# Kernel tuning notes

Measured on AMD Instinct MI355X. Metric: run time of the kernel, lower is better.

Reference implementation:

```python
import jax, jax.numpy as jnp
import numpy as np

B, L, D = 2, 4096, 1024
H, DK, DV = 4, 256, 256
CONV_K = 4
FIR_KS = (1, 3, 7, 15)
GQP = 128
NS = len(FIR_KS) + 2  # fir scales + delta path + direct value path
GIN = GQP + NS
GH = max(8, GIN)
CHUNK = 32
FLOOR = 0.02  # step 0 -> floor_start


def l2norm(x):
    return x * jax.lax.rsqrt(jnp.sum(x * x, -1, keepdims=True) + 1e-6)


def dw_causal_conv(x, w):
    # x: (B, L, C), w: (C, K) depthwise causal conv (ShortConvolution / FIR)
    K = w.shape[1]
    y = jax.lax.conv_general_dilated(
        jnp.moveaxis(x, 1, 2), w[:, None, :], (1,), [(K - 1, 0)],
        feature_group_count=w.shape[0],
        dimension_numbers=("NCH", "OIH", "NCH"))
    return jnp.moveaxis(y, 1, 2)


def delta_rule_chunkwise(q, k, v, beta):
    # q,k: (b,h,L,dk)  v: (b,h,L,dv)  beta: (b,h,L);  L % CHUNK == 0
    b, h, Lp, dk = q.shape
    dv = v.shape[-1]
    n = Lp // CHUNK
    q = l2norm(q)
    k = l2norm(k)
    v = v * beta[..., None]
    kb = k * beta[..., None]
    rs = lambda t: t.reshape(b, h, n, CHUNK, -1)
    q, k, v, kb = rs(q), rs(k), rs(v), rs(kb)
    tri = jnp.triu(jnp.ones((CHUNK, CHUNK), bool), 0)       # incl diag
    tri_s = jnp.triu(jnp.ones((CHUNK, CHUNK), bool), 1)     # strict upper
    # inv = -(k_beta k^T) masked to strictly-lower
    inv = -jnp.where(tri, 0.0, jnp.einsum('bhncd,bhned->bhnce', kb, k))
    # forward substitution: (I - A)^{-1} - I for strictly lower A
    for i in range(1, CHUNK):
        row = inv[:, :, :, i, :]                              # (b,h,n,C)
        upd = jnp.einsum('bhnk,bhnkj->bhnj', row, inv)        # zero for j>=i
        inv = inv.at[:, :, :, i, :].add(upd)
    inv = inv + jnp.eye(CHUNK, dtype=inv.dtype)
    inv = inv.astype(jnp.bfloat16).astype(q.dtype)
    u = inv @ v                                               # (b,h,n,C,dv)
    w = inv @ kb                                              # (b,h,n,C,dk)
    mv = lambda t: jnp.moveaxis(t, 2, 0)                      # -> (n,b,h,C,d)
    S0 = jnp.zeros((b, h, dk, dv), q.dtype)

    def step(S, xs):
        q_i, k_i, u_i, w_i = xs
        attn = jnp.where(tri_s, 0.0, q_i @ jnp.swapaxes(k_i, -1, -2))
        u_t = u_i - w_i @ S
        o = q_i @ S + attn @ u_t
        S = S + jnp.swapaxes(k_i, -1, -2) @ u_t
        return S, o

    _, out = jax.lax.scan(step, S0, (mv(q), mv(k), mv(u), mv(w)))
    return jnp.moveaxis(out, 0, 2).reshape(b, h, Lp, dv)


def rmsnorm(x, w, eps=1e-5):
    return x * jax.lax.rsqrt(jnp.mean(x * x, -1, keepdims=True) + eps) * w


def _dirac_fir(key, channels, k):
    w = jnp.zeros((channels, k), jnp.float32).at[:, -1].set(1.0)
    return w + 0.01 * jax.random.normal(key, (channels, k), jnp.float32)


def setup_inputs():
    key = jax.random.key(0)
    ks = jax.random.split(key, 24)
    sc = 0.02
    C = H * DV
    b2 = jnp.zeros((NS,), jnp.float32).at[-1].set(1.0)  # identity-path bias
    return {
        "hidden_states": jax.random.normal(ks[0], (B, L, D), jnp.float32),
        "Wq": jax.random.normal(ks[1], (D, H * DK), jnp.float32) * sc,
        "Wk": jax.random.normal(ks[2], (D, H * DK), jnp.float32) * sc,
        "Wv": jax.random.normal(ks[3], (D, H * DV), jnp.float32) * sc,
        "Wb": jax.random.normal(ks[4], (D, H), jnp.float32) * sc,
        "conv_q_w": jax.random.normal(ks[5], (H * DK, CONV_K), jnp.float32) * 0.1,
        "conv_k_w": jax.random.normal(ks[6], (H * DK, CONV_K), jnp.float32) * 0.1,
        "conv_v_w": jax.random.normal(ks[7], (H * DV, CONV_K), jnp.float32) * 0.1,
        "fir_w0": _dirac_fir(ks[8], C, FIR_KS[0]),
        "fir_w1": _dirac_fir(ks[9], C, FIR_KS[1]),
        "fir_w2": _dirac_fir(ks[10], C, FIR_KS[2]),
        "fir_w3": _dirac_fir(ks[11], C, FIR_KS[3]),
        "Wqg": jax.random.normal(ks[12], (D, GQP), jnp.float32) * sc,
        "bqg": jnp.zeros((GQP,), jnp.float32),
        "Wf1": jax.random.normal(ks[13], (GIN, GH), jnp.float32) * sc,
        "bf1": jnp.zeros((GH,), jnp.float32),
        "Wf2": jax.random.normal(ks[14], (GH, NS), jnp.float32) * sc,
        "bf2": b2,
        "log_temp": jnp.zeros((H,), jnp.float32),
        "o_norm_w": jnp.ones((DV,), jnp.float32),
        "Wo": jax.random.normal(ks[15], (H * DV, D), jnp.float32) * sc,
    }


def reference(hidden_states, Wq, Wk, Wv, Wb, conv_q_w, conv_k_w, conv_v_w,
              fir_w0, fir_w1, fir_w2, fir_w3, Wqg, bqg, Wf1, bf1, Wf2, bf2,
              log_temp, o_norm_w, Wo):
    x = hidden_states
    # projections + causal ShortConvolution with SiLU (qk_activation='silu')
    q = jax.nn.silu(dw_causal_conv(x @ Wq, conv_q_w))
    k = jax.nn.silu(dw_causal_conv(x @ Wk, conv_k_w))
    v = jax.nn.silu(dw_causal_conv(x @ Wv, conv_v_w))
    q = q.reshape(B, L, H, DK)
    k = k.reshape(B, L, H, DK)
    v_direct = v.reshape(B, L, H, DV)
    beta = jax.nn.sigmoid(x @ Wb)  # (B,L,H)
    bh = lambda t: jnp.swapaxes(t, 1, 2)  # (B,L,H,d) -> (B,H,L,d)
    delta_bh = delta_rule_chunkwise(bh(q), bh(k), bh(v_direct), jnp.swapaxes(beta, 1, 2))
    delta_out = jnp.swapaxes(delta_bh, 1, 2)  # (B,L,H,DV)
    # multi-scale depthwise causal FIR branches on the value stream
    v_flat = v_direct.reshape(B, L, H * DV)
    firs = [dw_causal_conv(v_flat, w).reshape(B, L, H, DV)
            for w in (fir_w0, fir_w1, fir_w2, fir_w3)]
    streams = jnp.stack(firs + [delta_out, v_direct], axis=3)  # (B,L,H,NS,DV)
    # query-conditioned summary router
    summaries = jnp.mean(streams, axis=-1)                     # (B,L,H,NS)
    qg = x @ Wqg + bqg                                         # (B,L,GQP)
    qg = jnp.broadcast_to(qg[:, :, None, :], (B, L, H, GQP))
    gate_in = jnp.concatenate([qg, summaries], axis=-1)        # (B,L,H,GIN)
    hmid = jax.nn.gelu(gate_in @ Wf1 + bf1, approximate=False)
    logits = (hmid @ Wf2 + bf2) / jnp.exp(log_temp)[None, None, :, None]
    p = jax.nn.softmax(logits, axis=-1)
    p = p * (1.0 - NS * FLOOR) + FLOOR                          # prob floor
    fused = jnp.einsum('blhs,blhsd->blhd', p, streams)
    o = rmsnorm(fused, o_norm_w)
    return o.reshape(B, L, H * DV) @ Wo
```

## Files before the change

kernel.cpp:

```cpp
#include <hip/hip_runtime.h>
#include <hip/hip_bf16.h>
#include <math.h>

#define B_ 2
#define L_ 4096
#define D_ 1024
#define H_ 4
#define DK_ 256
#define BL_ 8192
#define C_ 1024
#define NCH_ 128
#define GQP_c 128
#define NS_c 6
#define GIN_c 134
#define GH_c 134

typedef __attribute__((ext_vector_type(8))) short short8;
typedef __attribute__((ext_vector_type(4))) float f32x4;

__device__ __forceinline__ float block_sum256(float v, float* red) {
  int t = threadIdx.x;
  #pragma unroll
  for (int o = 32; o > 0; o >>= 1) v += __shfl_down(v, o, 64);
  __syncthreads();
  if ((t & 63) == 0) red[t >> 6] = v;
  __syncthreads();
  return red[0] + red[1] + red[2] + red[3];
}

__device__ __forceinline__ unsigned short bf16bits(float f) {
  __hip_bfloat16 h = __float2bfloat16(f);
  return *(unsigned short*)&h;
}

__device__ __forceinline__ float bits2f(unsigned short u) {
  unsigned int x = ((unsigned int)u) << 16;
  return *(float*)&x;
}

__device__ __forceinline__ float4 fma4(float4 a, float4 b, float4 c) {
  return make_float4(fmaf(a.x, b.x, c.x), fmaf(a.y, b.y, c.y),
                     fmaf(a.z, b.z, c.z), fmaf(a.w, b.w, c.w));
}

__device__ __forceinline__ void gload_lds16(const void* g, void* l) {
  __builtin_amdgcn_global_load_lds(
      (const __attribute__((address_space(1))) void*)g,
      (__attribute__((address_space(3))) void*)l, 16, 0, 0);
}

__global__ __launch_bounds__(256) void f32_to_bf16_k(const float* __restrict__ in,
    __hip_bfloat16* __restrict__ out) {
  size_t i = ((size_t)blockIdx.x * 256 + threadIdx.x) << 2;
  float4 v = *(const float4*)(in + i);
  ushort4 o;
  o.x = bf16bits(v.x); o.y = bf16bits(v.y); o.z = bf16bits(v.z); o.w = bf16bits(v.w);
  *(ushort4*)((unsigned short*)out + i) = o;
}

__global__ __launch_bounds__(256) void transpose_bf16(const float* __restrict__ W,
    __hip_bfloat16* __restrict__ WT, int K, int N) {
  __shared__ float tile[32][33];
  int t = threadIdx.x;
  int r = t >> 3, c4 = (t & 7) << 2;
  int n0 = blockIdx.x << 5, k0 = blockIdx.y << 5;
  float4 v = *(const float4*)(W + (size_t)(k0 + r) * N + n0 + c4);
  tile[r][c4] = v.x; tile[r][c4 + 1] = v.y; tile[r][c4 + 2] = v.z; tile[r][c4 + 3] = v.w;
  __syncthreads();
  ushort4 o;
  o.x = bf16bits(tile[c4][r]);
  o.y = bf16bits(tile[c4 + 1][r]);
  o.z = bf16bits(tile[c4 + 2][r]);
  o.w = bf16bits(tile[c4 + 3][r]);
  *(ushort4*)((unsigned short*)WT + (size_t)(n0 + r) * K + k0 + c4) = o;
}

__global__ __launch_bounds__(256) void small_transpose(const float* __restrict__ in,
    float* __restrict__ out, int R, int Cc, int OS) {
  int total = Cc * OS;
  for (int e = blockIdx.x * 256 + threadIdx.x; e < total; e += gridDim.x * 256) {
    int cIdx = e / OS, r = e - cIdx * OS;
    out[e] = (r < R) ? in[(size_t)r * Cc + cIdx] : 0.f;
  }
}

__global__ __launch_bounds__(256) void wf1q_prep(const float* __restrict__ Wf1,
    __hip_bfloat16* __restrict__ out) {
  int idx = blockIdx.x * 256 + threadIdx.x;
  int u = idx >> 7, i = idx & 127;
  float val = (u < GH_c) ? Wf1[i * GH_c + u] : 0.f;
  out[idx] = __float2bfloat16(val);
}

__global__ __launch_bounds__(256) void gemm_bf16(
    const __hip_bfloat16* __restrict__ A, const __hip_bfloat16* __restrict__ BT,
    const float* __restrict__ bias, float* __restrict__ C, int M, int N, int K) {
  __shared__ __align__(16) __hip_bfloat16 Asm[4096];
  __shared__ __align__(16) __hip_bfloat16 Bsm[4096];
  int tid = threadIdx.x;
  int lane = tid & 63, wave = tid >> 6;
  int wm = wave >> 1, wn = wave & 1;
  int rowBase = blockIdx.y * 128, colBase = blockIdx.x * 128;
  f32x4 acc[4][4];
  #pragma unroll
  for (int i = 0; i < 4; ++i)
    #pragma unroll
    for (int j = 0; j < 4; ++j) acc[i][j] = (f32x4){0.f, 0.f, 0.f, 0.f};

  for (int kt = 0; kt < K; kt += 32) {
    __syncthreads();
    #pragma unroll
    for (int it = 0; it < 2; ++it) {
      int s = tid + (it << 8);
      int T = s >> 6, q = (s >> 4) & 3, m = s & 15;
      const __hip_bfloat16* ga = A + (size_t)(rowBase + T * 16 + m) * K + kt + q * 8;
      gload_lds16(ga, Asm + s * 8);
      const __hip_bfloat16* gb = BT + (size_t)(colBase + T * 16 + m) * K + kt + q * 8;
      gload_lds16(gb, Bsm + s * 8);
    }
    __syncthreads();
    short8 af[4], bfr[4];
    #pragma unroll
    for (int i = 0; i < 4; ++i) {
      af[i]  = *(const short8*)(Asm + ((wm * 4 + i) << 9) + lane * 8);
      bfr[i] = *(const short8*)(Bsm + ((wn * 4 + i) << 9) + lane * 8);
    }
    #pragma unroll
    for (int i = 0; i < 4; ++i)
      #pragma unroll
      for (int j = 0; j < 4; ++j)
        acc[i][j] = __builtin_amdgcn_mfma_f32_16x16x32_bf16(af[i], bfr[j], acc[i][j], 0, 0, 0);
  }
  int r0 = (lane >> 4) * 4, c0 = lane & 15;
  #pragma unroll
  for (int i = 0; i < 4; ++i) {
    int row = rowBase + (wm * 4 + i) * 16 + r0;
    #pragma unroll
    for (int j = 0; j < 4; ++j) {
      int col = colBase + (wn * 4 + j) * 16 + c0;
      float bs = bias ? bias[col] : 0.f;
      #pragma unroll
      for (int r = 0; r < 4; ++r)
        C[(size_t)(row + r) * N + col] = acc[i][j][r] + bs;
    }
  }
}

__global__ __launch_bounds__(256) void conv_silu(const float* __restrict__ in,
    const float* __restrict__ w, float* __restrict__ out) {
  int idx = blockIdx.x * 256 + threadIdx.x;
  int c = idx & (C_ - 1);
  int l = (idx >> 10) & (L_ - 1);
  float acc = 0.f;
  #pragma unroll
  for (int j = 0; j < 4; ++j) {
    int ll = l - 3 + j;
    if (ll >= 0) acc += w[(c << 2) + j] * in[idx + ((j - 3) << 10)];
  }
  out[idx] = acc / (1.f + expf(-acc));
}

__global__ __launch_bounds__(256) void beta_kernel(const float* __restrict__ x,
    const float* __restrict__ Wb, float* __restrict__ beta) {
  int row = blockIdx.x;
  int t = threadIdx.x;
  int h = t >> 6, lane = t & 63;
  const float* xr = x + (size_t)row * D_;
  float acc = 0.f;
  for (int k = lane; k < D_; k += 64) acc += xr[k] * Wb[(k << 2) + h];
  #pragma unroll
  for (int o = 32; o > 0; o >>= 1) acc += __shfl_down(acc, o, 64);
  if (lane == 0) beta[(row << 2) + h] = 1.f / (1.f + expf(-acc));
}

__global__ __launch_bounds__(256) void precompute(const float* __restrict__ q,
    const float* __restrict__ k, const float* __restrict__ v,
    const float* __restrict__ beta,
    float* __restrict__ qn, float* __restrict__ kn,
    float* __restrict__ vb, float* __restrict__ kb) {
  __shared__ float red[4];
  int bid = blockIdx.x;
  int t = threadIdx.x;
  int b = bid >> 14;
  int h = (bid >> 12) & 3;
  int l = bid & (L_ - 1);
  size_t in_off = (((size_t)(b * L_ + l)) << 10) + (h << 8) + t;
  float qv = q[in_off], kv = k[in_off], vv = v[in_off];
  float sq = block_sum256(qv * qv, red);
  float sk = block_sum256(kv * kv, red);
  float rq = rsqrtf(sq + 1e-6f);
  float rk = rsqrtf(sk + 1e-6f);
  float bt = beta[((b * L_ + l) << 2) + h];
  size_t oo = ((size_t)bid << 8) + t;
  float knv = kv * rk;
  qn[oo] = qv * rq;
  kn[oo] = knv;
  vb[oo] = vv * bt;
  kb[oo] = knv * bt;
}

__global__ __launch_bounds__(256) void inv_attn(const float* __restrict__ qn,
    const float* kn, const float* __restrict__ kb,
    float* __restrict__ invb, __hip_bfloat16* __restrict__ att_bf,
    __hip_bfloat16* knT_bf) {
  __shared__ float kn_s[32][257];
  __shared__ float inv_s[32][33];
  int ci = blockIdx.x;
  int t = threadIdx.x;
  size_t base = ((size_t)ci) << 13;
  for (int e = t; e < 8192; e += 256) kn_s[e >> 8][e & 255] = kn[base + e];
  __syncthreads();
  {
    unsigned short tmp[32];
    #pragma unroll
    for (int j = 0; j < 32; ++j) tmp[j] = bf16bits(kn_s[j][t]);
    unsigned short* kd = (unsigned short*)knT_bf + (((size_t)ci) << 14) +
                         (size_t)(t >> 4) * 512 + (size_t)(t & 15) * 8;
    #pragma unroll
    for (int g = 0; g < 4; ++g) *(uint4*)(kd + g * 128) = ((const uint4*)tmp)[g];
  }
  {
    int r = t >> 3, kt = t & 7;
    const float4* qrow = (const float4*)(qn + base + (size_t)r * 256 + (kt << 5));
    unsigned short tmp[32];
    #pragma unroll
    for (int i = 0; i < 8; ++i) {
      float4 f = qrow[i];
      tmp[i * 4 + 0] = bf16bits(f.x); tmp[i * 4 + 1] = bf16bits(f.y);
      tmp[i * 4 + 2] = bf16bits(f.z); tmp[i * 4 + 3] = bf16bits(f.w);
    }
    unsigned short* qd = (unsigned short*)knT_bf + (((size_t)ci) << 14) + 8192 +
                         (size_t)(((r >> 4) << 3) + kt) * 512 + (size_t)(r & 15) * 8;
    #pragma unroll
    for (int g = 0; g < 4; ++g) *(uint4*)(qd + g * 128) = ((const uint4*)tmp)[g];
  }
  #pragma unroll
  for (int p = 0; p < 4; ++p) {
    int e = t + (p << 8);
    int i = e >> 5, j = e & 31;
    const float* kbi = kb + base + (i << 8);
    const float* qni = qn + base + (i << 8);
    float am = 0.f, aa = 0.f;
    for (int kk = 0; kk < 256; ++kk) {
      float knv = kn_s[j][kk];
      am += kbi[kk] * knv;
      aa += qni[kk] * knv;
    }
    inv_s[i][j] = (j < i) ? -am : 0.f;
    ((unsigned short*)att_bf)[((size_t)ci << 10) + (size_t)(i >> 4) * 512 +
        (size_t)((i & 15) + ((j >> 3) << 4)) * 8 + (j & 7)] =
        bf16bits((j <= i) ? aa : 0.f);
  }
  __syncthreads();
  for (int i = 1; i < 32; ++i) {
    float upd = 0.f;
    if (t < i) {
      for (int kk = t + 1; kk < i; ++kk) upd += inv_s[i][kk] * inv_s[kk][t];
    }
    __syncthreads();
    if (t < i) inv_s[i][t] += upd;
    __syncthreads();
  }
  #pragma unroll
  for (int p = 0; p < 4; ++p) {
    int e = t + (p << 8);
    int i = e >> 5, j = e & 31;
    float val = inv_s[i][j] + (i == j ? 1.f : 0.f);
    val = __bfloat162float(__float2bfloat16(val));
    invb[((size_t)ci << 10) + e] = val;
  }
}

__global__ __launch_bounds__(256) void uw_kernel(const float* __restrict__ invb,
    float* __restrict__ vb_u, float* kb_w, __hip_bfloat16* w_bf) {
  __shared__ float inv_s[32][33];
  __shared__ float tile[32][260];
  int ci = blockIdx.x, t = threadIdx.x;
  size_t base = ((size_t)ci) << 13;
  for (int e = t; e < 1024; e += 256) inv_s[e >> 5][e & 31] = invb[((size_t)ci << 10) + e];
  for (int ph = 0; ph < 2; ++ph) {
    const float* src = (ph == 0) ? vb_u : kb_w;
    __syncthreads();
    for (int f = t; f < 2048; f += 256) {
      int e = f << 2;
      *(float4*)&tile[e >> 8][e & 255] = *(const float4*)(src + base + e);
    }
    __syncthreads();
    int c4 = (t & 63) << 2;
    int ig = t >> 6;
    float4 acc[8];
    #pragma unroll
    for (int ii = 0; ii < 8; ++ii) acc[ii] = make_float4(0.f, 0.f, 0.f, 0.f);
    for (int j = 0; j < 32; ++j) {
      float4 v4 = *(const float4*)&tile[j][c4];
      #pragma unroll
      for (int ii = 0; ii < 8; ++ii) {
        float iv = inv_s[(ig << 3) + ii][j];
        acc[ii].x += iv * v4.x; acc[ii].y += iv * v4.y;
        acc[ii].z += iv * v4.z; acc[ii].w += iv * v4.w;
      }
    }
    #pragma unroll
    for (int ii = 0; ii < 8; ++ii) {
      int i = (ig << 3) + ii;
      if (ph == 0) {
        *(float4*)(vb_u + base + (i << 8) + c4) = acc[ii];
      } else {
        ushort4 o;
        o.x = bf16bits(-acc[ii].x); o.y = bf16bits(-acc[ii].y);
        o.z = bf16bits(-acc[ii].z); o.w = bf16bits(-acc[ii].w);
        unsigned short* wd = (unsigned short*)w_bf + (((size_t)ci) << 14) +
            (size_t)(((i >> 4) << 3) + (c4 >> 5)) * 512 +
            (size_t)((i & 15) + (((c4 >> 3) & 3) << 4)) * 8 + (c4 & 7);
        *(ushort4*)wd = o;
      }
    }
  }
}

__global__ __launch_bounds__(128, 1) void scan_kernel(
    const __hip_bfloat16* __restrict__ w_bf,
    const __hip_bfloat16* __restrict__ kq_bf,
    const __hip_bfloat16* __restrict__ att_bf,
    const float* __restrict__ u, float* __restrict__ dout) {
  __shared__ __align__(16) unsigned short stg[2][25600];
  __shared__ __align__(16) unsigned short Shi[16 * 264];
  __shared__ __align__(16) unsigned short Slo[16 * 264];
  __shared__ __align__(16) float UtT[16 * 36];
  int tid = threadIdx.x;
  int wave = tid >> 6, lane = tid & 63;
  int mlane = lane & 15, quad = lane >> 4;
  int bh = blockIdx.x & 7;
  int cb = blockIdx.x >> 3;
  int cbase = cb << 4;

  const unsigned short* wbase = (const unsigned short*)w_bf;
  const unsigned short* kqbase = (const unsigned short*)kq_bf;
  const unsigned short* abase = (const unsigned short*)att_bf;

  auto stage_chunk = [&](int nc, int buf) {
    size_t ci = (size_t)(bh * NCH_ + nc);
    const unsigned short* wg = wbase + (ci << 14) + lane * 8;
    const unsigned short* kg = kqbase + (ci << 14) + lane * 8;
    const unsigned short* qg = kqbase + (ci << 14) + 8192 + lane * 8;
    const unsigned short* ag = abase + (ci << 10) + lane * 8;
    unsigned short* l = &stg[buf][lane * 8];
    #pragma unroll
    for (int s = 0; s < 16; ++s) {
      gload_lds16(wg + s * 512, l + s * 512);
      gload_lds16(kg + s * 512, l + 8192 + s * 512);
      gload_lds16(qg + s * 512, l + 16384 + s * 512);
    }
    gload_lds16(ag, l + 24576);
    gload_lds16(ag + 512, l + 25088);
  };
  float ur[8], urn[8];
  auto load_u8 = [&](int nc, float* dst) {
    size_t cbf = ((size_t)(bh * NCH_ + nc)) << 13;
    const float* up = u + cbf + (size_t)(quad * 4) * 256 + cbase + mlane;
    #pragma unroll
    for (int tt = 0; tt < 2; ++tt)
      #pragma unroll
      for (int r = 0; r < 4; ++r) dst[tt * 4 + r] = up[(tt * 16 + r) * 256];
  };

  f32x4 accS[16];
  if (wave == 1) {
    stage_chunk(0, 0);
    asm volatile("s_waitcnt vmcnt(0)" ::: "memory");
  } else {
    for (int e = lane; e < 16 * 264; e += 64) { Shi[e] = 0; Slo[e] = 0; }
    #pragma unroll
    for (int i = 0; i < 16; ++i) accS[i] = (f32x4){0.f, 0.f, 0.f, 0.f};
    load_u8(0, ur);
  }
  __syncthreads();

  for (int nc = 0; nc < NCH_; ++nc) {
    int cur = nc & 1;
    if (wave == 1) {
      if (nc + 1 < NCH_) stage_chunk(nc + 1, cur ^ 1);
      asm volatile("s_waitcnt vmcnt(0)" ::: "memory");
    } else {
      int nn = nc + 1 < NCH_ ? nc + 1 : NCH_ - 1;
      const unsigned short* SW = &stg[cur][0];
      const unsigned short* SK = &stg[cur][8192];
      const unsigned short* SQ = &stg[cur][16384];
      const unsigned short* SA = &stg[cur][24576];

      f32x4 uh0 = (f32x4){ur[0], ur[1], ur[2], ur[3]};
      f32x4 uh1 = (f32x4){ur[4], ur[5], ur[6], ur[7]};
      f32x4 ul0 = (f32x4){0.f, 0.f, 0.f, 0.f}, ul1 = (f32x4){0.f, 0.f, 0.f, 0.f};
      f32x4 oh0 = (f32x4){0.f, 0.f, 0.f, 0.f}, oh1 = (f32x4){0.f, 0.f, 0.f, 0.f};
      f32x4 ol0 = (f32x4){0.f, 0.f, 0.f, 0.f}, ol1 = (f32x4){0.f, 0.f, 0.f, 0.f};
      #pragma unroll
      for (int kt = 0; kt < 8; ++kt) {
        short8 bhi = *(const short8*)&Shi[mlane * 264 + kt * 32 + quad * 8];
        short8 blo = *(const short8*)&Slo[mlane * 264 + kt * 32 + quad * 8];
        short8 w0 = *(const short8*)&SW[kt * 512 + lane * 8];
        short8 w1 = *(const short8*)&SW[(8 + kt) * 512 + lane * 8];
        short8 q0 = *(const short8*)&SQ[kt * 512 + lane * 8];
        short8 q1 = *(const short8*)&SQ[(8 + kt) * 512 + lane * 8];
        uh0 = __builtin_amdgcn_mfma_f32_16x16x32_bf16(w0, bhi, uh0, 0, 0, 0);
        ul0 = __builtin_amdgcn_mfma_f32_16x16x32_bf16(w0, blo, ul0, 0, 0, 0);
        uh1 = __builtin_amdgcn_mfma_f32_16x16x32_bf16(w1, bhi, uh1, 0, 0, 0);
        ul1 = __builtin_amdgcn_mfma_f32_16x16x32_bf16(w1, blo, ul1, 0, 0, 0);
        oh0 = __builtin_amdgcn_mfma_f32_16x16x32_bf16(q0, bhi, oh0, 0, 0, 0);
        ol0 = __builtin_amdgcn_mfma_f32_16x16x32_bf16(q0, blo, ol0, 0, 0, 0);
        oh1 = __builtin_amdgcn_mfma_f32_16x16x32_bf16(q1, bhi, oh1, 0, 0, 0);
        ol1 = __builtin_amdgcn_mfma_f32_16x16x32_bf16(q1, blo, ol1, 0, 0, 0);
      }
      f32x4 ut0 = uh0 + ul0, ut1 = uh1 + ul1;
      *(f32x4*)&UtT[mlane * 36 + quad * 4] = ut0;
      *(f32x4*)&UtT[mlane * 36 + 16 + quad * 4] = ut1;
      load_u8(nn, urn);
      short8 but;
      {
        const float* up = &UtT[mlane * 36 + quad * 8];
        #pragma unroll
        for (int j = 0; j < 8; ++j) but[j] = (short)bf16bits(up[j]);
      }
      short8 a0 = *(const short8*)&SA[lane * 8];
      short8 a1 = *(const short8*)&SA[512 + lane * 8];
      f32x4 o0 = oh0 + ol0, o1 = oh1 + ol1;
      o0 = __builtin_amdgcn_mfma_f32_16x16x32_bf16(a0, but, o0, 0, 0, 0);
      o1 = __builtin_amdgcn_mfma_f32_16x16x32_bf16(a1, but, o1, 0, 0, 0);
      size_t cbf = ((size_t)(bh * NCH_ + nc)) << 13;
      float* op = dout + cbf + (size_t)(quad * 4) * 256 + cbase + mlane;
      #pragma unroll
      for (int r = 0; r < 4; ++r) { op[r * 256] = o0[r]; op[(16 + r) * 256] = o1[r]; }
      #pragma unroll
      for (int t2 = 0; t2 < 16; ++t2) {
        short8 kA = *(const short8*)&SK[t2 * 512 + lane * 8];
        accS[t2] = __builtin_amdgcn_mfma_f32_16x16x32_bf16(kA, but, accS[t2], 0, 0, 0);
        unsigned short nh[4], nl[4];
        #pragma unroll
        for (int r = 0; r < 4; ++r) {
          float sv = accS[t2][r];
          unsigned short hb = bf16bits(sv);
          nh[r] = hb;
          nl[r] = bf16bits(sv - bits2f(hb));
        }
        *(uint2*)&Shi[mlane * 264 + t2 * 16 + quad * 4] = *(const uint2*)nh;
        *(uint2*)&Slo[mlane * 264 + t2 * 16 + quad * 4] = *(const uint2*)nl;
      }
      #pragma unroll
      for (int r = 0; r < 8; ++r) ur[r] = urn[r];
    }
    __syncthreads();
  }
}

__global__ __launch_bounds__(256, 1) void gate_kernel(
    const float* __restrict__ v, const float* __restrict__ delta,
    const float* __restrict__ qgH,
    const float* __restrict__ fw0, const float* __restrict__ fw1T,
    const float* __restrict__ fw2T, const float* __restrict__ fw3T,
    const float* __restrict__ Wf1, const float* __restrict__ Wf2,
    const float* __restrict__ bf1, const float* __restrict__ bf2,
    const float* __restrict__ ltm, const float* __restrict__ onw,
    __hip_bfloat16* __restrict__ obf) {
  __shared__ float W1t[6][136];
  __shared__ float W2f[804];
  __shared__ float bf1s[136];
  int t = threadIdx.x;
  int wave = t >> 6, lane = t & 63;
  for (int e = t; e < 804; e += 256) {
    int s = e / 134, u = e - s * 134;
    W1t[s][u] = Wf1[(128 + s) * GH_c + u];
    W2f[e] = Wf2[e];
  }
  if (t < GH_c) bf1s[t] = bf1[t];
  __syncthreads();

  int bid = blockIdx.x;
  int bl0 = (((bid & 7) << 7) | (bid >> 3)) << 3;
  int b = bl0 >> 12;
  int h = wave;
  int c = (h << 8) + (lane << 2);

  float4 fw3r[15], fw2r[7], fw1r[3], fw0r;
  #pragma unroll
  for (int j = 0; j < 15; ++j) fw3r[j] = *(const float4*)(fw3T + (j << 10) + c);
  #pragma unroll
  for (int j = 0; j < 7; ++j) fw2r[j] = *(const float4*)(fw2T + (j << 10) + c);
  #pragma unroll
  for (int j = 0; j < 3; ++j) fw1r[j] = *(const float4*)(fw1T + (j << 10) + c);
  fw0r = *(const float4*)(fw0 + c);
  float4 ow = *(const float4*)(onw + (lane << 2));
  float itemp = expf(ltm[h]);
  float b2r[6];
  #pragma unroll
  for (int s = 0; s < 6; ++s) b2r[s] = bf2[s];
  int u3 = 128 + (lane < 6 ? lane : 0);

  auto gelu = [](float a) -> float {
    return 0.5f * a * (1.f + erff(a * 0.70710678f));
  };

  for (int tk = 0; tk < 8; ++tk) {
    int bl = bl0 + tk;
    int l = bl & (L_ - 1);
    float4 st0, st1, st2, st3, st4, st5;
    st1 = make_float4(0, 0, 0, 0);
    st2 = make_float4(0, 0, 0, 0);
    st3 = make_float4(0, 0, 0, 0);
    #pragma unroll
    for (int j = 0; j < 15; ++j) {
      int ll = l - 14 + j;
      float4 vj = make_float4(0, 0, 0, 0);
      if (ll >= 0) vj = *(const float4*)(v + ((((size_t)(b * L_ + ll)) << 10) + c));
      st3 = fma4(fw3r[j], vj, st3);
      if (j >= 8) st2 = fma4(fw2r[j - 8], vj, st2);
      if (j >= 12) st1 = fma4(fw1r[j - 12], vj, st1);
      if (j == 14) {
        st0 = make_float4(fw0r.x * vj.x, fw0r.y * vj.y, fw0r.z * vj.z, fw0r.w * vj.w);
        st5 = vj;
      }
    }
    st4 = *(const float4*)(delta + ((((size_t)((b * H_ + h) * L_ + l)) << 8) + (lane << 2)));

    float s0 = st0.x + st0.y + st0.z + st0.w;
    float s1 = st1.x + st1.y + st1.z + st1.w;
    float s2 = st2.x + st2.y + st2.z + st2.w;
    float s3 = st3.x + st3.y + st3.z + st3.w;
    float s4 = st4.x + st4.y + st4.z + st4.w;
    float s5 = st5.x + st5.y + st5.z + st5.w;
    #pragma unroll
    for (int o = 32; o > 0; o >>= 1) {
      s0 += __shfl_down(s0, o, 64); s1 += __shfl_down(s1, o, 64);
      s2 += __shfl_down(s2, o, 64); s3 += __shfl_down(s3, o, 64);
      s4 += __shfl_down(s4, o, 64); s5 += __shfl_down(s5, o, 64);
    }
    float ss_[6];
    ss_[0] = __shfl(s0, 0, 64) * (1.f / 256.f);
    ss_[1] = __shfl(s1, 0, 64) * (1.f / 256.f);
    ss_[2] = __shfl(s2, 0, 64) * (1.f / 256.f);
    ss_[3] = __shfl(s3, 0, 64) * (1.f / 256.f);
    ss_[4] = __shfl(s4, 0, 64) * (1.f / 256.f);
    ss_[5] = __shfl(s5, 0, 64) * (1.f / 256.f);

    const float* qr = qgH + ((size_t)bl << 8);
    float a0 = qr[lane] + bf1s[lane];
    float a1 = qr[64 + lane] + bf1s[64 + lane];
    float a2 = qr[u3] + bf1s[u3];
    #pragma unroll
    for (int s = 0; s < 6; ++s) {
      a0 = fmaf(W1t[s][lane], ss_[s], a0);
      a1 = fmaf(W1t[s][64 + lane], ss_[s], a1);
      a2 = fmaf(W1t[s][u3], ss_[s], a2);
    }
    float h0 = gelu(a0);
    float h1 = gelu(a1);
    float h2 = (lane < 6) ? gelu(a2) : 0.f;

    const float* w2a = W2f + lane * 6;
    const float* w2b = W2f + (64 + lane) * 6;
    const float* w2c = W2f + u3 * 6;
    float t0 = h0 * w2a[0] + h1 * w2b[0] + h2 * w2c[0];
    float t1 = h0 * w2a[1] + h1 * w2b[1] + h2 * w2c[1];
    float t2 = h0 * w2a[2] + h1 * w2b[2] + h2 * w2c[2];
    float t3 = h0 * w2a[3] + h1 * w2b[3] + h2 * w2c[3];
    float t4 = h0 * w2a[4] + h1 * w2b[4] + h2 * w2c[4];
    float t5 = h0 * w2a[5] + h1 * w2b[5] + h2 * w2c[5];
    #pragma unroll
    for (int o = 32; o > 0; o >>= 1) {
      t0 += __shfl_down(t0, o, 64); t1 += __shfl_down(t1, o, 64);
      t2 += __shfl_down(t2, o, 64); t3 += __shfl_down(t3, o, 64);
      t4 += __shfl_down(t4, o, 64); t5 += __shfl_down(t5, o, 64);
    }
    float p0, p1, p2, p3, p4, p5;
    if (lane == 0) {
      float l0v = (t0 + b2r[0]) / itemp, l1v = (t1 + b2r[1]) / itemp;
      float l2v = (t2 + b2r[2]) / itemp, l3v = (t3 + b2r[3]) / itemp;
      float l4v = (t4 + b2r[4]) / itemp, l5v = (t5 + b2r[5]) / itemp;
      float m = fmaxf(fmaxf(fmaxf(l0v, l1v), fmaxf(l2v, l3v)), fmaxf(l4v, l5v));
      float e0 = expf(l0v - m), e1 = expf(l1v - m), e2 = expf(l2v - m);
      float e3 = expf(l3v - m), e4 = expf(l4v - m), e5 = expf(l5v - m);
      float inv = 1.f / (e0 + e1 + e2 + e3 + e4 + e5);
      p0 = e0 * inv * 0.88f + 0.02f; p1 = e1 * inv * 0.88f + 0.02f;
      p2 = e2 * inv * 0.88f + 0.02f; p3 = e3 * inv * 0.88f + 0.02f;
      p4 = e4 * inv * 0.88f + 0.02f; p5 = e5 * inv * 0.88f + 0.02f;
    }
    p0 = __shfl(p0, 0, 64); p1 = __shfl(p1, 0, 64); p2 = __shfl(p2, 0, 64);
    p3 = __shfl(p3, 0, 64); p4 = __shfl(p4, 0, 64); p5 = __shfl(p5, 0, 64);

    float4 fu;
    fu.x = p0 * st0.x + p1 * st1.x + p2 * st2.x + p3 * st3.x + p4 * st4.x + p5 * st5.x;
    fu.y = p0 * st0.y + p1 * st1.y + p2 * st2.y + p3 * st3.y + p4 * st4.y + p5 * st5.y;
    fu.z = p0 * st0.z + p1 * st1.z + p2 * st2.z + p3 * st3.z + p4 * st4.z + p5 * st5.z;
    fu.w = p0 * st0.w + p1 * st1.w + p2 * st2.w + p3 * st3.w + p4 * st4.w + p5 * st5.w;
    float ssq = fu.x * fu.x + fu.y * fu.y + fu.z * fu.z + fu.w * fu.w;
    #pragma unroll
    for (int o = 32; o > 0; o >>= 1) ssq += __shfl_xor(ssq, o, 64);
    float sc = rsqrtf(ssq * (1.f / 256.f) + 1e-5f);
    ushort4 ob;
    ob.x = bf16bits(fu.x * sc * ow.x);
    ob.y = bf16bits(fu.y * sc * ow.y);
    ob.z = bf16bits(fu.z * sc * ow.z);
    ob.w = bf16bits(fu.w * sc * ow.w);
    *(ushort4*)((unsigned short*)obf + (((size_t)bl) << 10) + c) = ob;
  }
}

extern "C" void kernel_launch(void* const* d_in, const int* in_sizes, int n_in,
                              void* d_out, int out_size, void* d_ws, size_t ws_size,
                              hipStream_t stream) {
  const float* x   = (const float*)d_in[0];
  const float* Wq  = (const float*)d_in[1];
  const float* Wk  = (const float*)d_in[2];
  const float* Wv  = (const float*)d_in[3];
  const float* Wb  = (const float*)d_in[4];
  const float* cqw = (const float*)d_in[5];
  const float* ckw = (const float*)d_in[6];
  const float* cvw = (const float*)d_in[7];
  const float* fw0 = (const float*)d_in[8];
  const float* fw1 = (const float*)d_in[9];
  const float* fw2 = (const float*)d_in[10];
  const float* fw3 = (const float*)d_in[11];
  const float* Wqg = (const float*)d_in[12];
  const float* bqg = (const float*)d_in[13];
  const float* Wf1 = (const float*)d_in[14];
  const float* bf1 = (const float*)d_in[15];
  const float* Wf2 = (const float*)d_in[16];
  const float* bf2 = (const float*)d_in[17];
  const float* ltm = (const float*)d_in[18];
  const float* onw = (const float*)d_in[19];
  const float* Wo  = (const float*)d_in[20];
  float* out = (float*)d_out;
  float* ws = (float*)d_ws;

  const size_t BIG = (size_t)BL_ * C_;
  float* qpre = ws;
  float* kpre = ws + BIG;
  float* vpre = ws + 2 * BIG;
  float* qs   = ws + 3 * BIG;
  float* ks   = ws + 4 * BIG;
  float* vs   = ws + 5 * BIG;
  float* kbw  = ws + 6 * BIG;
  float* invb = ws + 7 * BIG;
  float* attb = invb + (size_t)1024 * 1024;
  float* beta = attb + (size_t)1024 * 1024;
  float* qg   = beta + (size_t)BL_ * H_;

  __hip_bfloat16* x_bf  = (__hip_bfloat16*)qs;
  __hip_bfloat16* wqT   = (__hip_bfloat16*)kbw;
  __hip_bfloat16* wkT   = wqT + (size_t)1024 * 1024;
  __hip_bfloat16* wvT   = wkT + (size_t)1024 * 1024;
  __hip_bfloat16* wqgT  = wvT + (size_t)1024 * 1024;
  __hip_bfloat16* woT   = (__hip_bfloat16*)kbw;
  __hip_bfloat16* gate_bf = (__hip_bfloat16*)qpre;
  __hip_bfloat16* knT_bf = (__hip_bfloat16*)kpre;
  __hip_bfloat16* w_bf   = (__hip_bfloat16*)kbw;
  __hip_bfloat16* att_bf = (__hip_bfloat16*)attb;
  float* scr   = attb + (size_t)600000;
  float* fw1T  = scr;
  float* fw2T  = scr + 3072;
  float* fw3T  = scr + 10240;

  float* qgH = ks;
  __hip_bfloat16* qg_bf  = (__hip_bfloat16*)(ks + (size_t)3 * 1024 * 1024);
  __hip_bfloat16* wf1qT  = (__hip_bfloat16*)(ks + (size_t)4 * 1024 * 1024);

  dim3 blk(256);
  f32_to_bf16_k<<<dim3(BL_ * D_ / 1024), blk, 0, stream>>>(x, x_bf);
  transpose_bf16<<<dim3(32, 32), blk, 0, stream>>>(Wq, wqT, D_, C_);
  transpose_bf16<<<dim3(32, 32), blk, 0, stream>>>(Wk, wkT, D_, C_);
  transpose_bf16<<<dim3(32, 32), blk, 0, stream>>>(Wv, wvT, D_, C_);
  transpose_bf16<<<dim3(4, 32), blk, 0, stream>>>(Wqg, wqgT, D_, GQP_c);
  small_transpose<<<dim3(16), blk, 0, stream>>>(fw1, fw1T, 1024, 3, 1024);
  small_transpose<<<dim3(32), blk, 0, stream>>>(fw2, fw2T, 1024, 7, 1024);
  small_transpose<<<dim3(64), blk, 0, stream>>>(fw3, fw3T, 1024, 15, 1024);
  gemm_bf16<<<dim3(8, 64), blk, 0, stream>>>(x_bf, wqT, nullptr, qpre, BL_, C_, D_);
  gemm_bf16<<<dim3(8, 64), blk, 0, stream>>>(x_bf, wkT, nullptr, kpre, BL_, C_, D_);
  gemm_bf16<<<dim3(8, 64), blk, 0, stream>>>(x_bf, wvT, nullptr, vpre, BL_, C_, D_);
  gemm_bf16<<<dim3(1, 64), blk, 0, stream>>>(x_bf, wqgT, bqg, qg, BL_, GQP_c, D_);
  beta_kernel<<<dim3(BL_), blk, 0, stream>>>(x, Wb, beta);
  conv_silu<<<dim3(BL_ * C_ / 256), blk, 0, stream>>>(qpre, cqw, qs);
  conv_silu<<<dim3(BL_ * C_ / 256), blk, 0, stream>>>(kpre, ckw, ks);
  conv_silu<<<dim3(BL_ * C_ / 256), blk, 0, stream>>>(vpre, cvw, vs);
  precompute<<<dim3(B_ * H_ * L_), blk, 0, stream>>>(qs, ks, vs, beta, qpre, kpre,
                                                     vpre, kbw);
  f32_to_bf16_k<<<dim3(BL_ * GQP_c / 1024), blk, 0, stream>>>(qg, qg_bf);
  wf1q_prep<<<dim3(128), blk, 0, stream>>>(Wf1, wf1qT);
  gemm_bf16<<<dim3(2, 64), blk, 0, stream>>>(qg_bf, wf1qT, nullptr, qgH, BL_, 256, 128);
  inv_attn<<<dim3(1024), blk, 0, stream>>>(qpre, kpre, kbw, invb, att_bf, knT_bf);
  uw_kernel<<<dim3(1024), blk, 0, stream>>>(invb, vpre, kbw, w_bf);
  scan_kernel<<<dim3(128), dim3(128), 0, stream>>>(w_bf, knT_bf, att_bf, vpre, qs);
  transpose_bf16<<<dim3(32, 32), blk, 0, stream>>>(Wo, woT, C_, D_);
  gate_kernel<<<dim3(1024), blk, 0, stream>>>(vs, qs, qgH, fw0, fw1T, fw2T, fw3T,
                                              Wf1, Wf2, bf1, bf2, ltm, onw, gate_bf);
  gemm_bf16<<<dim3(8, 64), blk, 0, stream>>>(gate_bf, woT, nullptr, out, BL_, D_, C_);
}
```

Before: 1.016 ms.

## Load W and Q chunk tiles directly into registers, stage only K and attn in LDS

In the scan kernel, the compute wave now prefetches the next chunk's W and Q operand fragments straight from global memory into registers (short8 Wr/Qr), instead of having the producer wave stage them through LDS. This shrinks the LDS staging buffers so the producer only copies K and the attention tile. Wave-specialised control flow is split into separate loops that synchronise with raw s_barrier, and the producer returns early. The change cuts LDS traffic and footprint on the serial recurrence path, at the cost of more VGPR pressure (32 short8 registers) and global-load latency that must hide behind the MFMA work.

```diff
diff --git a/kernel.cpp b/kernel.cpp
--- a/kernel.cpp
+++ b/kernel.cpp
@@ -323,7 +323,7 @@
     const __hip_bfloat16* __restrict__ kq_bf,
     const __hip_bfloat16* __restrict__ att_bf,
     const float* __restrict__ u, float* __restrict__ dout) {
-  __shared__ __align__(16) unsigned short stg[2][25600];
+  __shared__ __align__(16) unsigned short stg[2][9216];
   __shared__ __align__(16) unsigned short Shi[16 * 264];
   __shared__ __align__(16) unsigned short Slo[16 * 264];
   __shared__ __align__(16) float UtT[16 * 36];
@@ -338,23 +338,39 @@
   const unsigned short* kqbase = (const unsigned short*)kq_bf;
   const unsigned short* abase = (const unsigned short*)att_bf;
 
-  auto stage_chunk = [&](int nc, int buf) {
-    size_t ci = (size_t)(bh * NCH_ + nc);
-    const unsigned short* wg = wbase + (ci << 14) + lane * 8;
-    const unsigned short* kg = kqbase + (ci << 14) + lane * 8;
-    const unsigned short* qg = kqbase + (ci << 14) + 8192 + lane * 8;
-    const unsigned short* ag = abase + (ci << 10) + lane * 8;
-    unsigned short* l = &stg[buf][lane * 8];
-    #pragma unroll
-    for (int s = 0; s < 16; ++s) {
-      gload_lds16(wg + s * 512, l + s * 512);
-      gload_lds16(kg + s * 512, l + 8192 + s * 512);
-      gload_lds16(qg + s * 512, l + 16384 + s * 512);
-    }
-    gload_lds16(ag, l + 24576);
-    gload_lds16(ag + 512, l + 25088);
+  if (wave == 1) {
+    auto stage_chunk = [&](int nc, int buf) {
+      size_t ci = (size_t)(bh * NCH_ + nc);
+      const unsigned short* kg = kqbase + (ci << 14) + lane * 8;
+      const unsigned short* ag = abase + (ci << 10) + lane * 8;
+      unsigned short* l = &stg[buf][lane * 8];
+      #pragma unroll
+      for (int s = 0; s < 16; ++s) gload_lds16(kg + s * 512, l + s * 512);
+      gload_lds16(ag, l + 8192);
+      gload_lds16(ag + 512, l + 8704);
+    };
+    stage_chunk(0, 0);
+    asm volatile("s_waitcnt vmcnt(0)" ::: "memory");
+    asm volatile("s_barrier" ::: "memory");
+    for (int nc = 0; nc < NCH_; ++nc) {
+      if (nc + 1 < NCH_) {
+        stage_chunk(nc + 1, (nc + 1) & 1);
+        asm volatile("s_waitcnt vmcnt(0)" ::: "memory");
+      }
+      asm volatile("s_barrier" ::: "memory");
+    }
+    return;
+  }
+
+  short8 Wr[16], Qr[16];
+  float ur[8], urn[8];
+  auto load_WQ = [&](int nc) {
+    size_t cb14 = ((size_t)(bh * NCH_ + nc)) << 14;
+    const short8* wg = (const short8*)(wbase + cb14 + (size_t)lane * 8);
+    const short8* qg = (const short8*)(kqbase + cb14 + 8192 + (size_t)lane * 8);
+    #pragma unroll
+    for (int s = 0; s < 16; ++s) { Wr[s] = wg[s * 64]; Qr[s] = qg[s * 64]; }
   };
-  float ur[8], urn[8];
   auto load_u8 = [&](int nc, float* dst) {
     size_t cbf = ((size_t)(bh * NCH_ + nc)) << 13;
     const float* up = u + cbf + (size_t)(quad * 4) * 256 + cbase + mlane;
@@ -364,90 +380,77 @@
       for (int r = 0; r < 4; ++r) dst[tt * 4 + r] = up[(tt * 16 + r) * 256];
   };
 
+  for (int e = lane; e < 16 * 264; e += 64) { Shi[e] = 0; Slo[e] = 0; }
   f32x4 accS[16];
-  if (wave == 1) {
-    stage_chunk(0, 0);
-    asm volatile("s_waitcnt vmcnt(0)" ::: "memory");
-  } else {
-    for (int e = lane; e < 16 * 264; e += 64) { Shi[e] = 0; Slo[e] = 0; }
-    #pragma unroll
-    for (int i = 0; i < 16; ++i) accS[i] = (f32x4){0.f, 0.f, 0.f, 0.f};
-    load_u8(0, ur);
-  }
-  __syncthreads();
+  #pragma unroll
+  for (int i = 0; i < 16; ++i) accS[i] = (f32x4){0.f, 0.f, 0.f, 0.f};
+  load_WQ(0);
+  load_u8(0, ur);
+  asm volatile("s_barrier" ::: "memory");
 
   for (int nc = 0; nc < NCH_; ++nc) {
     int cur = nc & 1;
-    if (wave == 1) {
-      if (nc + 1 < NCH_) stage_chunk(nc + 1, cur ^ 1);
-      asm volatile("s_waitcnt vmcnt(0)" ::: "memory");
-    } else {
-      int nn = nc + 1 < NCH_ ? nc + 1 : NCH_ - 1;
-      const unsigned short* SW = &stg[cur][0];
-      const unsigned short* SK = &stg[cur][8192];
-      const unsigned short* SQ = &stg[cur][16384];
-      const unsigned short* SA = &stg[cur][24576];
-
-      f32x4 uh0 = (f32x4){ur[0], ur[1], ur[2], ur[3]};
-      f32x4 uh1 = (f32x4){ur[4], ur[5], ur[6], ur[7]};
-      f32x4 ul0 = (f32x4){0.f, 0.f, 0.f, 0.f}, ul1 = (f32x4){0.f, 0.f, 0.f, 0.f};
-      f32x4 oh0 = (f32x4){0.f, 0.f, 0.f, 0.f}, oh1 = (f32x4){0.f, 0.f, 0.f, 0.f};
-      f32x4 ol0 = (f32x4){0.f, 0.f, 0.f, 0.f}, ol1 = (f32x4){0.f, 0.f, 0.f, 0.f};
+    int nn = nc + 1 < NCH_ ? nc + 1 : NCH_ - 1;
+    const unsigned short* SK = &stg[cur][0];
+    const unsigned short* SA = &stg[cur][8192];
+    short8 a0 = *(const short8*)&SA[lane * 8];
+    short8 a1 = *(const short8*)&SA[512 + lane * 8];
+
+    f32x4 uh0 = (f32x4){ur[0], ur[1], ur[2], ur[3]};
+    f32x4 uh1 = (f32x4){ur[4], ur[5], ur[6], ur[7]};
+    f32x4 ul0 = (f32x4){0.f, 0.f, 0.f, 0.f}, ul1 = (f32x4){0.f, 0.f, 0.f, 0.f};
+    f32x4 oh0 = (f32x4){0.f, 0.f, 0.f, 0.f}, oh1 = (f32x4){0.f, 0.f, 0.f, 0.f};
+    f32x4 ol0 = (f32x4){0.f, 0.f, 0.f, 0.f}, ol1 = (f32x4){0.f, 0.f, 0.f, 0.f};
+    #pragma unroll
+    for (int kt = 0; kt < 8; ++kt) {
+      short8 bhi = *(const short8*)&Shi[mlane * 264 + kt * 32 + quad * 8];
+      short8 blo = *(const short8*)&Slo[mlane * 264 + kt * 32 + quad * 8];
+      uh0 = __builtin_amdgcn_mfma_f32_16x16x32_bf16(Wr[kt], bhi, uh0, 0, 0, 0);
+      ul0 = __builtin_amdgcn_mfma_f32_16x16x32_bf16(Wr[kt], blo, ul0, 0, 0, 0);
+      uh1 = __builtin_amdgcn_mfma_f32_16x16x32_bf16(Wr[8 + kt], bhi, uh1, 0, 0, 0);
+      ul1 = __builtin_amdgcn_mfma_f32_16x16x32_bf16(Wr[8 + kt], blo, ul1, 0, 0, 0);
+      oh0 = __builtin_amdgcn_mfma_f32_16x16x32_bf16(Qr[kt], bhi, oh0, 0, 0, 0);
+      ol0 = __builtin_amdgcn_mfma_f32_16x16x32_bf16(Qr[kt], blo, ol0, 0, 0, 0);
+      oh1 = __builtin_amdgcn_mfma_f32_16x16x32_bf16(Qr[8 + kt], bhi, oh1, 0, 0, 0);
+      ol1 = __builtin_amdgcn_mfma_f32_16x16x32_bf16(Qr[8 + kt], blo, ol1, 0, 0, 0);
+    }
+    f32x4 ut0 = uh0 + ul0, ut1 = uh1 + ul1;
+    *(f32x4*)&UtT[mlane * 36 + quad * 4] = ut0;
+    *(f32x4*)&UtT[mlane * 36 + 16 + quad * 4] = ut1;
+    load_WQ(nn);
+    load_u8(nn, urn);
+    __builtin_amdgcn_sched_barrier(0);
+    short8 but;
+    {
+      const float* up = &UtT[mlane * 36 + quad * 8];
       #pragma unroll
-      for (int kt = 0; kt < 8; ++kt) {
-        short8 bhi = *(const short8*)&Shi[mlane * 264 + kt * 32 + quad * 8];
-        short8 blo = *(const short8*)&Slo[mlane * 264 + kt * 32 + quad * 8];
-        short8 w0 = *(const short8*)&SW[kt * 512 + lane * 8];
-        short8 w1 = *(const short8*)&SW[(8 + kt) * 512 + lane * 8];
-        short8 q0 = *(const short8*)&SQ[kt * 512 + lane * 8];
-        short8 q1 = *(const short8*)&SQ[(8 + kt) * 512 + lane * 8];
-        uh0 = __builtin_amdgcn_mfma_f32_16x16x32_bf16(w0, bhi, uh0, 0, 0, 0);
-        ul0 = __builtin_amdgcn_mfma_f32_16x16x32_bf16(w0, blo, ul0, 0, 0, 0);
-        uh1 = __builtin_amdgcn_mfma_f32_16x16x32_bf16(w1, bhi, uh1, 0, 0, 0);
-        ul1 = __builtin_amdgcn_mfma_f32_16x16x32_bf16(w1, blo, ul1, 0, 0, 0);
-        oh0 = __builtin_amdgcn_mfma_f32_16x16x32_bf16(q0, bhi, oh0, 0, 0, 0);
-        ol0 = __builtin_amdgcn_mfma_f32_16x16x32_bf16(q0, blo, ol0, 0, 0, 0);
-        oh1 = __builtin_amdgcn_mfma_f32_16x16x32_bf16(q1, bhi, oh1, 0, 0, 0);
-        ol1 = __builtin_amdgcn_mfma_f32_16x16x32_bf16(q1, blo, ol1, 0, 0, 0);
+      for (int j = 0; j < 8; ++j) but[j] = (short)bf16bits(up[j]);
+    }
+    f32x4 o0 = oh0 + ol0, o1 = oh1 + ol1;
+    o0 = __builtin_amdgcn_mfma_f32_16x16x32_bf16(a0, but, o0, 0, 0, 0);
+    o1 = __builtin_amdgcn_mfma_f32_16x16x32_bf16(a1, but, o1, 0, 0, 0);
+    size_t cbf = ((size_t)(bh * NCH_ + nc)) << 13;
+    float* op = dout + cbf + (size_t)(quad * 4) * 256 + cbase + mlane;
+    #pragma unroll
+    for (int r = 0; r < 4; ++r) { op[r * 256] = o0[r]; op[(16 + r) * 256] = o1[r]; }
+    #pragma unroll
+    for (int t2 = 0; t2 < 16; ++t2) {
+      short8 kA = *(const short8*)&SK[t2 * 512 + lane * 8];
+      accS[t2] = __builtin_amdgcn_mfma_f32_16x16x32_bf16(kA, but, accS[t2], 0, 0, 0);
+      unsigned short nh[4], nl[4];
+      #pragma unroll
+      for (int r = 0; r < 4; ++r) {
+        float sv = accS[t2][r];
+        unsigned short hb = bf16bits(sv);
+        nh[r] = hb;
+        nl[r] = bf16bits(sv - bits2f(hb));
       }
-      f32x4 ut0 = uh0 + ul0, ut1 = uh1 + ul1;
-      *(f32x4*)&UtT[mlane * 36 + quad * 4] = ut0;
-      *(f32x4*)&UtT[mlane * 36 + 16 + quad * 4] = ut1;
-      load_u8(nn, urn);
-      short8 but;
-      {
-        const float* up = &UtT[mlane * 36 + quad * 8];
-        #pragma unroll
-        for (int j = 0; j < 8; ++j) but[j] = (short)bf16bits(up[j]);
-      }
-      short8 a0 = *(const short8*)&SA[lane * 8];
-      short8 a1 = *(const short8*)&SA[512 + lane * 8];
-      f32x4 o0 = oh0 + ol0, o1 = oh1 + ol1;
-      o0 = __builtin_amdgcn_mfma_f32_16x16x32_bf16(a0, but, o0, 0, 0, 0);
-      o1 = __builtin_amdgcn_mfma_f32_16x16x32_bf16(a1, but, o1, 0, 0, 0);
-      size_t cbf = ((size_t)(bh * NCH_ + nc)) << 13;
-      float* op = dout + cbf + (size_t)(quad * 4) * 256 + cbase + mlane;
-      #pragma unroll
-      for (int r = 0; r < 4; ++r) { op[r * 256] = o0[r]; op[(16 + r) * 256] = o1[r]; }
-      #pragma unroll
-      for (int t2 = 0; t2 < 16; ++t2) {
-        short8 kA = *(const short8*)&SK[t2 * 512 + lane * 8];
-        accS[t2] = __builtin_amdgcn_mfma_f32_16x16x32_bf16(kA, but, accS[t2], 0, 0, 0);
-        unsigned short nh[4], nl[4];
-        #pragma unroll
-        for (int r = 0; r < 4; ++r) {
-          float sv = accS[t2][r];
-          unsigned short hb = bf16bits(sv);
-          nh[r] = hb;
-          nl[r] = bf16bits(sv - bits2f(hb));
-        }
-        *(uint2*)&Shi[mlane * 264 + t2 * 16 + quad * 4] = *(const uint2*)nh;
-        *(uint2*)&Slo[mlane * 264 + t2 * 16 + quad * 4] = *(const uint2*)nl;
-      }
-      #pragma unroll
-      for (int r = 0; r < 8; ++r) ur[r] = urn[r];
-    }
-    __syncthreads();
+      *(uint2*)&Shi[mlane * 264 + t2 * 16 + quad * 4] = *(const uint2*)nh;
+      *(uint2*)&Slo[mlane * 264 + t2 * 16 + quad * 4] = *(const uint2*)nl;
+    }
+    #pragma unroll
+    for (int r = 0; r < 8; ++r) ur[r] = urn[r];
+    asm volatile("s_barrier" ::: "memory");
   }
 }
 
```

New measurement: 1.082 ms. +6.5%, slower.
